# Performance work log

Measured on AMD Instinct MI355X. Metric: run time of the kernel, lower is better.

## Reference

```python
import jax, jax.numpy as jnp
import numpy as np

N_NODES = 100000
IN_DIM = 500
HID_DIM = 128
OUT_DIM = 40
N_EDGES = 1600000


def setup_inputs() -> dict:
    key = jax.random.key(0)
    k1, k2, k3, k4, k5 = jax.random.split(key, 5)
    x = jax.random.normal(k1, (N_NODES, IN_DIM), dtype=jnp.float32)
    edge_index = jax.random.randint(k2, (2, N_EDGES), 0, N_NODES, dtype=jnp.int64)
    # Glorot-style init for linear weights, zero bias (as in PyG GCNConv)
    W1 = jax.random.normal(k3, (IN_DIM, HID_DIM), dtype=jnp.float32) / np.sqrt(IN_DIM)
    b1 = jnp.zeros((HID_DIM,), dtype=jnp.float32)
    W2 = jax.random.normal(k4, (HID_DIM, OUT_DIM), dtype=jnp.float32) / np.sqrt(HID_DIM)
    b2 = jnp.zeros((OUT_DIM,), dtype=jnp.float32)
    return {"x": x, "edge_index": edge_index, "W1": W1, "b1": b1, "W2": W2, "b2": b2}


def reference(x, edge_index, W1, b1, W2, b2):
    N = x.shape[0]
    # GCNConv: add self-loops, symmetric normalization deg^-1/2 A deg^-1/2
    loops = jnp.arange(N, dtype=edge_index.dtype)
    src = jnp.concatenate([edge_index[0], loops])  # [E+N]
    dst = jnp.concatenate([edge_index[1], loops])  # [E+N]
    deg = jax.ops.segment_sum(jnp.ones_like(dst, dtype=x.dtype), dst, num_segments=N)
    dinv = jnp.where(deg > 0, jax.lax.rsqrt(deg), 0.0)
    norm = (dinv[src] * dinv[dst])[:, None]  # [E+N, 1]

    def gcn_conv(h, W, b):
        h = h @ W                              # [N, F_out] linear first (PyG order)
        msg = h[src] * norm                    # gather + scale: [E+N, F_out]
        agg = jax.ops.segment_sum(msg, dst, num_segments=N)  # scatter-add
        return agg + b

    h = jax.nn.relu(gcn_conv(x, W1, b1))
    # dropout(p=0.5) is identity in eval mode
    h = gcn_conv(h, W2, b2)
    return jax.nn.log_softmax(h, axis=1)
```

## Files before the change

kernel.cpp:

```cpp
#include <hip/hip_runtime.h>
#include <hip/hip_bf16.h>

#define IN_DIM 500
#define HID 128
#define OUTD 40
#define KPAD 512

typedef __bf16 bf16x8 __attribute__((ext_vector_type(8)));
typedef float f32x16 __attribute__((ext_vector_type(16)));

static __device__ __forceinline__ float rsqrt_acc(float x) {
  float r = rsqrtf(x);
  return r * (1.5f - 0.5f * x * r * r);
}

static __device__ __forceinline__ unsigned short bf16_of(float f) {
  __bf16 h = (__bf16)f;
  return __builtin_bit_cast(unsigned short, h);
}
static __device__ __forceinline__ float bf16_back(unsigned short u) {
  return (float)__builtin_bit_cast(__bf16, u);
}

__global__ void zero_kernel(int* __restrict__ p, int n) {
  int i = blockIdx.x * 256 + threadIdx.x;
  if (i < n) p[i] = 0;
}

__global__ void hist_kernel(const int* __restrict__ dst, int* __restrict__ deg, int E) {
  int e = blockIdx.x * 256 + threadIdx.x;
  if (e < E) atomicAdd(&deg[dst[e]], 1);
}

__global__ void dinv_kernel(const int* __restrict__ deg, float* __restrict__ dinv, int N) {
  int n = blockIdx.x * 256 + threadIdx.x;
  if (n < N) dinv[n] = rsqrt_acc((float)deg[n] + 1.0f);
}

__global__ void scan_a(const int* __restrict__ deg, int* __restrict__ partial,
                       int* __restrict__ blockSums, int N) {
  __shared__ int sums[256];
  int t = threadIdx.x;
  int base = blockIdx.x * 1024 + t * 4;
  int v0 = (base + 0) < N ? deg[base + 0] : 0;
  int v1 = (base + 1) < N ? deg[base + 1] : 0;
  int v2 = (base + 2) < N ? deg[base + 2] : 0;
  int v3 = (base + 3) < N ? deg[base + 3] : 0;
  int l0 = v0, l1 = l0 + v1, l2 = l1 + v2, l3 = l2 + v3;
  sums[t] = l3;
  __syncthreads();
  for (int o = 1; o < 256; o <<= 1) {
    int a = sums[t];
    int b = (t >= o) ? sums[t - o] : 0;
    __syncthreads();
    sums[t] = a + b;
    __syncthreads();
  }
  int excl = sums[t] - l3;
  if (t == 0) blockSums[blockIdx.x] = sums[255];
  if (base + 0 < N) partial[base + 0] = excl;
  if (base + 1 < N) partial[base + 1] = excl + l0;
  if (base + 2 < N) partial[base + 2] = excl + l1;
  if (base + 3 < N) partial[base + 3] = excl + l2;
}

__global__ void scan_b(int* __restrict__ blockSums, int nb) {
  __shared__ int s[256];
  int t = threadIdx.x;
  int orig = (t < nb) ? blockSums[t] : 0;
  s[t] = orig;
  __syncthreads();
  for (int o = 1; o < 256; o <<= 1) {
    int a = s[t];
    int b = (t >= o) ? s[t - o] : 0;
    __syncthreads();
    s[t] = a + b;
    __syncthreads();
  }
  if (t < nb) blockSums[t] = s[t] - orig;
}

__global__ void scan_c(int* __restrict__ row_ptr, const int* __restrict__ blockOff,
                       int* __restrict__ cursor, int N, int E) {
  int n = blockIdx.x * 256 + threadIdx.x;
  if (n < N) {
    int v = row_ptr[n] + blockOff[n >> 10];
    row_ptr[n] = v;
    cursor[n] = v;
  }
  if (n == 0 && blockIdx.x == 0) row_ptr[N] = E;
}

__global__ void place_kernel(const int* __restrict__ src, const int* __restrict__ dst,
                             const float* __restrict__ dinv, int* __restrict__ cursor,
                             int2* __restrict__ ePair, int E) {
  int e = blockIdx.x * 256 + threadIdx.x;
  if (e < E) {
    int s = src[e], d = dst[e];
    int pos = atomicAdd(&cursor[d], 1);
    int2 rec;
    rec.x = s;
    rec.y = __float_as_int(dinv[s] * dinv[d]);
    ePair[pos] = rec;
  }
}

__global__ void convW1_kernel(const float* __restrict__ W1, unsigned short* __restrict__ Whi,
                              unsigned short* __restrict__ Wlo) {
  int idx = blockIdx.x * 256 + threadIdx.x;
  if (idx >= HID * KPAD) return;
  int n = idx >> 9, k = idx & (KPAD - 1);
  float f = (k < IN_DIM) ? W1[(size_t)k * HID + n] : 0.f;
  unsigned short h = bf16_of(f);
  Whi[idx] = h;
  Wlo[idx] = bf16_of(f - bf16_back(h));
}

#define LSTR 40

__global__ __launch_bounds__(256) void gemm1_kernel(const float* __restrict__ X,
                                                    const unsigned short* __restrict__ Whi,
                                                    const unsigned short* __restrict__ Wlo,
                                                    float* __restrict__ H1, int N) {
  __shared__ unsigned short sAhi[64 * LSTR];
  __shared__ unsigned short sAlo[64 * LSTR];
  __shared__ unsigned short sBhi[128 * LSTR];
  __shared__ unsigned short sBlo[128 * LSTR];
  const int t = threadIdx.x;
  const int rowBase = blockIdx.x * 64;
  const int lane = t & 63;
  const int w = t >> 6;
  const int rw = w & 1;
  const int cw = w >> 1;
  const int m = lane & 31;
  const int quad = lane >> 5;

  f32x16 acc[2];
  acc[0] = (f32x16)(0.f);
  acc[1] = (f32x16)(0.f);

  const int arow = t >> 2;
  const int akoff = (t & 3) * 8;
  const bool arok = (rowBase + arow) < N;
  const float* xrow = X + (size_t)(rowBase + (arok ? arow : 0)) * IN_DIM;
  const int brow = t >> 1;
  const int bkoff = (t & 1) * 16;

  for (int k0 = 0; k0 < KPAD; k0 += 32) {
    __syncthreads();
    {
      float f[8];
      if (arok && (k0 + akoff + 8) <= IN_DIM) {
        const float4* p = (const float4*)(xrow + k0 + akoff);
        float4 v0 = p[0], v1 = p[1];
        f[0] = v0.x; f[1] = v0.y; f[2] = v0.z; f[3] = v0.w;
        f[4] = v1.x; f[5] = v1.y; f[6] = v1.z; f[7] = v1.w;
      } else {
#pragma unroll
        for (int j = 0; j < 8; j++) {
          int k = k0 + akoff + j;
          f[j] = (arok && k < IN_DIM) ? xrow[k] : 0.f;
        }
      }
#pragma unroll
      for (int g = 0; g < 2; g++) {
        ushort4 h, l;
        h.x = bf16_of(f[g*4+0]); l.x = bf16_of(f[g*4+0] - bf16_back(h.x));
        h.y = bf16_of(f[g*4+1]); l.y = bf16_of(f[g*4+1] - bf16_back(h.y));
        h.z = bf16_of(f[g*4+2]); l.z = bf16_of(f[g*4+2] - bf16_back(h.z));
        h.w = bf16_of(f[g*4+3]); l.w = bf16_of(f[g*4+3] - bf16_back(h.w));
        *(ushort4*)&sAhi[arow * LSTR + akoff + g * 4] = h;
        *(ushort4*)&sAlo[arow * LSTR + akoff + g * 4] = l;
      }
    }
    {
      const size_t gb = (size_t)brow * KPAD + k0 + bkoff;
      uint4 h0 = *(const uint4*)&Whi[gb];
      uint4 h1v = *(const uint4*)&Whi[gb + 8];
      uint4 l0 = *(const uint4*)&Wlo[gb];
      uint4 l1 = *(const uint4*)&Wlo[gb + 8];
      *(uint4*)&sBhi[brow * LSTR + bkoff] = h0;
      *(uint4*)&sBhi[brow * LSTR + bkoff + 8] = h1v;
      *(uint4*)&sBlo[brow * LSTR + bkoff] = l0;
      *(uint4*)&sBlo[brow * LSTR + bkoff + 8] = l1;
    }
    __syncthreads();

#pragma unroll
    for (int sub = 0; sub < 2; sub++) {
      const int ks = sub * 16 + quad * 8;
      bf16x8 ah = *(const bf16x8*)&sAhi[(rw * 32 + m) * LSTR + ks];
      bf16x8 al = *(const bf16x8*)&sAlo[(rw * 32 + m) * LSTR + ks];
#pragma unroll
      for (int nt = 0; nt < 2; nt++) {
        bf16x8 bhv = *(const bf16x8*)&sBhi[(cw * 64 + nt * 32 + m) * LSTR + ks];
        bf16x8 blv = *(const bf16x8*)&sBlo[(cw * 64 + nt * 32 + m) * LSTR + ks];
        acc[nt] = __builtin_amdgcn_mfma_f32_32x32x16_bf16(ah, bhv, acc[nt], 0, 0, 0);
        acc[nt] = __builtin_amdgcn_mfma_f32_32x32x16_bf16(ah, blv, acc[nt], 0, 0, 0);
        acc[nt] = __builtin_amdgcn_mfma_f32_32x32x16_bf16(al, bhv, acc[nt], 0, 0, 0);
      }
    }
  }

#pragma unroll
  for (int nt = 0; nt < 2; nt++) {
#pragma unroll
    for (int r = 0; r < 16; r++) {
      int rowin = (r & 3) + 8 * (r >> 2) + 4 * quad;
      int grow = rowBase + rw * 32 + rowin;
      if (grow < N) H1[(size_t)grow * HID + cw * 64 + nt * 32 + m] = acc[nt][r];
    }
  }
}

__global__ void agg1_kernel(const float* __restrict__ h1, const int* __restrict__ row_ptr,
                            const int2* __restrict__ ePair, const float* __restrict__ dinv,
                            const float* __restrict__ b1, float* __restrict__ hrelu, int N) {
  int gid = blockIdx.x * 256 + threadIdx.x;
  int n = gid >> 5, c4 = (gid & 31) * 4;
  if (n >= N) return;
  float di = dinv[n];
  float sl = di * di;
  float4 acc = *(const float4*)&h1[(size_t)n * HID + c4];
  acc.x *= sl; acc.y *= sl; acc.z *= sl; acc.w *= sl;
  int i = row_ptr[n];
  const int s1 = row_ptr[n + 1];
  for (; i + 4 <= s1; i += 4) {
    int2 e0 = ePair[i], e1 = ePair[i + 1], e2 = ePair[i + 2], e3 = ePair[i + 3];
    float w0 = __int_as_float(e0.y), w1 = __int_as_float(e1.y);
    float w2 = __int_as_float(e2.y), w3 = __int_as_float(e3.y);
    float4 v0 = *(const float4*)&h1[(size_t)e0.x * HID + c4];
    float4 v1 = *(const float4*)&h1[(size_t)e1.x * HID + c4];
    float4 v2 = *(const float4*)&h1[(size_t)e2.x * HID + c4];
    float4 v3 = *(const float4*)&h1[(size_t)e3.x * HID + c4];
    acc.x += w0 * v0.x + w1 * v1.x + w2 * v2.x + w3 * v3.x;
    acc.y += w0 * v0.y + w1 * v1.y + w2 * v2.y + w3 * v3.y;
    acc.z += w0 * v0.z + w1 * v1.z + w2 * v2.z + w3 * v3.z;
    acc.w += w0 * v0.w + w1 * v1.w + w2 * v2.w + w3 * v3.w;
  }
  for (; i < s1; i++) {
    int2 e = ePair[i];
    float w = __int_as_float(e.y);
    float4 v = *(const float4*)&h1[(size_t)e.x * HID + c4];
    acc.x += w * v.x; acc.y += w * v.y; acc.z += w * v.z; acc.w += w * v.w;
  }
  float4 bb = *(const float4*)&b1[c4];
  float4 r;
  r.x = fmaxf(acc.x + bb.x, 0.f);
  r.y = fmaxf(acc.y + bb.y, 0.f);
  r.z = fmaxf(acc.z + bb.z, 0.f);
  r.w = fmaxf(acc.w + bb.w, 0.f);
  *(float4*)&hrelu[(size_t)n * HID + c4] = r;
}

__global__ __launch_bounds__(256) void gemm2_kernel(const float* __restrict__ A,
                                                    const float* __restrict__ W2,
                                                    float* __restrict__ H2, int N) {
  __shared__ float tA[64 * 129];
  __shared__ float w2s[128 * 48];
  const int t = threadIdx.x;
  const int rowBase = blockIdx.x * 64;
  for (int idx = t; idx < 128 * 48; idx += 256) {
    int k = idx / 48, c = idx - k * 48;
    w2s[idx] = (c < OUTD) ? W2[k * OUTD + c] : 0.f;
  }
  for (int f = t; f < 2048; f += 256) {
    int row = f >> 5, c4 = (f & 31) * 4;
    float4 v = make_float4(0.f, 0.f, 0.f, 0.f);
    if (rowBase + row < N) v = *(const float4*)&A[(size_t)(rowBase + row) * HID + c4];
    tA[row * 129 + c4 + 0] = v.x;
    tA[row * 129 + c4 + 1] = v.y;
    tA[row * 129 + c4 + 2] = v.z;
    tA[row * 129 + c4 + 3] = v.w;
  }
  __syncthreads();
  const int row = t >> 2;
  const int c0 = (t & 3) * 12;
  float acc[12];
#pragma unroll
  for (int j = 0; j < 12; j++) acc[j] = 0.f;
  for (int k = 0; k < HID; k++) {
    float a = tA[row * 129 + k];
    const float* bp = &w2s[k * 48 + c0];
#pragma unroll
    for (int j = 0; j < 12; j++) acc[j] += a * bp[j];
  }
  int r = rowBase + row;
  if (r < N) {
#pragma unroll
    for (int j = 0; j < 12; j++) {
      int c = c0 + j;
      if (c < OUTD) H2[(size_t)r * OUTD + c] = acc[j];
    }
  }
}

__global__ void agg2_kernel(const float* __restrict__ h2, const int* __restrict__ row_ptr,
                            const int2* __restrict__ ePair, const float* __restrict__ dinv,
                            const float* __restrict__ b2, float* __restrict__ out, int N) {
  int gid = blockIdx.x * 256 + threadIdx.x;
  int n = gid / 10;
  int c4 = (gid - n * 10) * 4;
  if (n >= N) return;
  float di = dinv[n];
  float sl = di * di;
  float4 acc = *(const float4*)&h2[(size_t)n * OUTD + c4];
  acc.x *= sl; acc.y *= sl; acc.z *= sl; acc.w *= sl;
  int i = row_ptr[n];
  const int s1 = row_ptr[n + 1];
  for (; i + 4 <= s1; i += 4) {
    int2 e0 = ePair[i], e1 = ePair[i + 1], e2 = ePair[i + 2], e3 = ePair[i + 3];
    float w0 = __int_as_float(e0.y), w1 = __int_as_float(e1.y);
    float w2 = __int_as_float(e2.y), w3 = __int_as_float(e3.y);
    float4 v0 = *(const float4*)&h2[(size_t)e0.x * OUTD + c4];
    float4 v1 = *(const float4*)&h2[(size_t)e1.x * OUTD + c4];
    float4 v2 = *(const float4*)&h2[(size_t)e2.x * OUTD + c4];
    float4 v3 = *(const float4*)&h2[(size_t)e3.x * OUTD + c4];
    acc.x += w0 * v0.x + w1 * v1.x + w2 * v2.x + w3 * v3.x;
    acc.y += w0 * v0.y + w1 * v1.y + w2 * v2.y + w3 * v3.y;
    acc.z += w0 * v0.z + w1 * v1.z + w2 * v2.z + w3 * v3.z;
    acc.w += w0 * v0.w + w1 * v1.w + w2 * v2.w + w3 * v3.w;
  }
  for (; i < s1; i++) {
    int2 e = ePair[i];
    float w = __int_as_float(e.y);
    float4 v = *(const float4*)&h2[(size_t)e.x * OUTD + c4];
    acc.x += w * v.x; acc.y += w * v.y; acc.z += w * v.z; acc.w += w * v.w;
  }
  float* o = &out[(size_t)n * OUTD + c4];
  o[0] = acc.x + b2[c4 + 0];
  o[1] = acc.y + b2[c4 + 1];
  o[2] = acc.z + b2[c4 + 2];
  o[3] = acc.w + b2[c4 + 3];
}

__global__ void lsm_kernel(float* __restrict__ out, int N) {
  int n = blockIdx.x * 256 + threadIdx.x;
  if (n >= N) return;
  float* row = out + (size_t)n * OUTD;
  float v[OUTD];
  float m = -3.4e38f;
#pragma unroll
  for (int j = 0; j < OUTD; j++) {
    v[j] = row[j];
    m = fmaxf(m, v[j]);
  }
  float s = 0.f;
#pragma unroll
  for (int j = 0; j < OUTD; j++) s += expf(v[j] - m);
  float lse = m + logf(s);
#pragma unroll
  for (int j = 0; j < OUTD; j++) row[j] = v[j] - lse;
}

extern "C" void kernel_launch(void* const* d_in, const int* in_sizes, int n_in,
                              void* d_out, int out_size, void* d_ws, size_t ws_size,
                              hipStream_t stream) {
  const float* x  = (const float*)d_in[0];
  const int*   ei = (const int*)d_in[1];
  const float* W1 = (const float*)d_in[2];
  const float* b1 = (const float*)d_in[3];
  const float* W2 = (const float*)d_in[4];
  const float* b2 = (const float*)d_in[5];
  float* out = (float*)d_out;

  const int N = in_sizes[0] / IN_DIM;
  const int E = in_sizes[1] / 2;
  const int* src = ei;
  const int* dst = ei + E;

  char* wsb = (char*)d_ws;
  size_t off = 0;
  auto alloc = [&](size_t bytes) -> char* {
    char* p = wsb + off;
    off = (off + bytes + 1023) & ~(size_t)1023;
    return p;
  };
  int*   deg       = (int*)alloc((size_t)N * 4);
  float* dinv      = (float*)alloc((size_t)N * 4);
  int*   blockSums = (int*)alloc(1024);
  int*   row_ptr   = (int*)alloc((size_t)(N + 1) * 4);
  int*   cursor    = (int*)alloc((size_t)N * 4);
  int2*  ePair     = (int2*)alloc((size_t)E * 8);
  unsigned short* Whi = (unsigned short*)alloc((size_t)HID * KPAD * 2);
  unsigned short* Wlo = (unsigned short*)alloc((size_t)HID * KPAD * 2);
  float* h1        = (float*)alloc((size_t)N * HID * 4);
  float* hrelu     = (float*)alloc((size_t)N * HID * 4);
  float* h2        = h1;
  (void)n_in; (void)out_size;

  if (off > ws_size) return;

  const int gE = (E + 255) / 256;
  const int gN = (N + 255) / 256;
  const int nb = (N + 1023) / 1024;

  zero_kernel<<<gN, 256, 0, stream>>>(deg, N);
  hist_kernel<<<gE, 256, 0, stream>>>(dst, deg, E);
  dinv_kernel<<<gN, 256, 0, stream>>>(deg, dinv, N);
  scan_a<<<nb, 256, 0, stream>>>(deg, row_ptr, blockSums, N);
  scan_b<<<1, 256, 0, stream>>>(blockSums, nb);
  scan_c<<<gN, 256, 0, stream>>>(row_ptr, blockSums, cursor, N, E);
  place_kernel<<<gE, 256, 0, stream>>>(src, dst, dinv, cursor, ePair, E);
  convW1_kernel<<<(HID * KPAD + 255) / 256, 256, 0, stream>>>(W1, Whi, Wlo);

  gemm1_kernel<<<(N + 63) / 64, 256, 0, stream>>>(x, Whi, Wlo, h1, N);
  agg1_kernel<<<(N * 32 + 255) / 256, 256, 0, stream>>>(h1, row_ptr, ePair, dinv, b1, hrelu, N);
  gemm2_kernel<<<(N + 63) / 64, 256, 0, stream>>>(hrelu, W2, h2, N);
  agg2_kernel<<<(N * 10 + 255) / 256, 256, 0, stream>>>(h2, row_ptr, ePair, dinv, b2, out, N);
  lsm_kernel<<<gN, 256, 0, stream>>>(out, N);
}
```

Measured before the change: 725.8 us.

## Store intermediate node features in fp16 to halve gather traffic

The intermediate activations h1, hrelu and h2 are now stored as fp16 instead of fp32, while accumulation stays in fp32. Agg1 is rewritten so each thread handles 8 fp16 channels, using 16 threads per node instead of 32. The aim is to halve the bytes moved by the random-gather aggregation kernels and by the GEMM stores and loads. The cost is reduced precision in intermediates, with fp16 range and rounding error that could matter for the tolerance check.

```diff
diff --git a/kernel.cpp b/kernel.cpp
--- a/kernel.cpp
+++ b/kernel.cpp
@@ -8,6 +8,8 @@
 
 typedef __bf16 bf16x8 __attribute__((ext_vector_type(8)));
 typedef float f32x16 __attribute__((ext_vector_type(16)));
+typedef unsigned short u16x8 __attribute__((ext_vector_type(8)));
+typedef unsigned short u16x4 __attribute__((ext_vector_type(4)));
 
 static __device__ __forceinline__ float rsqrt_acc(float x) {
   float r = rsqrtf(x);
@@ -20,6 +22,13 @@
 }
 static __device__ __forceinline__ float bf16_back(unsigned short u) {
   return (float)__builtin_bit_cast(__bf16, u);
+}
+static __device__ __forceinline__ unsigned short h16_of(float f) {
+  _Float16 h = (_Float16)f;
+  return __builtin_bit_cast(unsigned short, h);
+}
+static __device__ __forceinline__ float h16_back(unsigned short u) {
+  return (float)__builtin_bit_cast(_Float16, u);
 }
 
 __global__ void zero_kernel(int* __restrict__ p, int n) {
@@ -121,7 +130,7 @@
 __global__ __launch_bounds__(256) void gemm1_kernel(const float* __restrict__ X,
                                                     const unsigned short* __restrict__ Whi,
                                                     const unsigned short* __restrict__ Wlo,
-                                                    float* __restrict__ H1, int N) {
+                                                    unsigned short* __restrict__ H1, int N) {
   __shared__ unsigned short sAhi[64 * LSTR];
   __shared__ unsigned short sAlo[64 * LSTR];
   __shared__ unsigned short sBhi[128 * LSTR];
@@ -208,54 +217,58 @@
     for (int r = 0; r < 16; r++) {
       int rowin = (r & 3) + 8 * (r >> 2) + 4 * quad;
       int grow = rowBase + rw * 32 + rowin;
-      if (grow < N) H1[(size_t)grow * HID + cw * 64 + nt * 32 + m] = acc[nt][r];
-    }
-  }
-}
-
-__global__ void agg1_kernel(const float* __restrict__ h1, const int* __restrict__ row_ptr,
+      if (grow < N) H1[(size_t)grow * HID + cw * 64 + nt * 32 + m] = h16_of(acc[nt][r]);
+    }
+  }
+}
+
+__global__ void agg1_kernel(const unsigned short* __restrict__ h1, const int* __restrict__ row_ptr,
                             const int2* __restrict__ ePair, const float* __restrict__ dinv,
-                            const float* __restrict__ b1, float* __restrict__ hrelu, int N) {
+                            const float* __restrict__ b1, unsigned short* __restrict__ hrelu, int N) {
   int gid = blockIdx.x * 256 + threadIdx.x;
-  int n = gid >> 5, c4 = (gid & 31) * 4;
+  int n = gid >> 4, c8 = (gid & 15) * 8;
   if (n >= N) return;
   float di = dinv[n];
   float sl = di * di;
-  float4 acc = *(const float4*)&h1[(size_t)n * HID + c4];
-  acc.x *= sl; acc.y *= sl; acc.z *= sl; acc.w *= sl;
+  float acc[8];
+  u16x8 sv = *(const u16x8*)&h1[(size_t)n * HID + c8];
+#pragma unroll
+  for (int j = 0; j < 8; j++) acc[j] = sl * h16_back(sv[j]);
   int i = row_ptr[n];
   const int s1 = row_ptr[n + 1];
   for (; i + 4 <= s1; i += 4) {
     int2 e0 = ePair[i], e1 = ePair[i + 1], e2 = ePair[i + 2], e3 = ePair[i + 3];
     float w0 = __int_as_float(e0.y), w1 = __int_as_float(e1.y);
     float w2 = __int_as_float(e2.y), w3 = __int_as_float(e3.y);
-    float4 v0 = *(const float4*)&h1[(size_t)e0.x * HID + c4];
-    float4 v1 = *(const float4*)&h1[(size_t)e1.x * HID + c4];
-    float4 v2 = *(const float4*)&h1[(size_t)e2.x * HID + c4];
-    float4 v3 = *(const float4*)&h1[(size_t)e3.x * HID + c4];
-    acc.x += w0 * v0.x + w1 * v1.x + w2 * v2.x + w3 * v3.x;
-    acc.y += w0 * v0.y + w1 * v1.y + w2 * v2.y + w3 * v3.y;
-    acc.z += w0 * v0.z + w1 * v1.z + w2 * v2.z + w3 * v3.z;
-    acc.w += w0 * v0.w + w1 * v1.w + w2 * v2.w + w3 * v3.w;
+    u16x8 v0 = *(const u16x8*)&h1[(size_t)e0.x * HID + c8];
+    u16x8 v1 = *(const u16x8*)&h1[(size_t)e1.x * HID + c8];
+    u16x8 v2 = *(const u16x8*)&h1[(size_t)e2.x * HID + c8];
+    u16x8 v3 = *(const u16x8*)&h1[(size_t)e3.x * HID + c8];
+#pragma unroll
+    for (int j = 0; j < 8; j++) {
+      acc[j] += w0 * h16_back(v0[j]) + w1 * h16_back(v1[j]) +
+                w2 * h16_back(v2[j]) + w3 * h16_back(v3[j]);
+    }
   }
   for (; i < s1; i++) {
     int2 e = ePair[i];
     float w = __int_as_float(e.y);
-    float4 v = *(const float4*)&h1[(size_t)e.x * HID + c4];
-    acc.x += w * v.x; acc.y += w * v.y; acc.z += w * v.z; acc.w += w * v.w;
-  }
-  float4 bb = *(const float4*)&b1[c4];
-  float4 r;
-  r.x = fmaxf(acc.x + bb.x, 0.f);
-  r.y = fmaxf(acc.y + bb.y, 0.f);
-  r.z = fmaxf(acc.z + bb.z, 0.f);
-  r.w = fmaxf(acc.w + bb.w, 0.f);
-  *(float4*)&hrelu[(size_t)n * HID + c4] = r;
-}
-
-__global__ __launch_bounds__(256) void gemm2_kernel(const float* __restrict__ A,
+    u16x8 v = *(const u16x8*)&h1[(size_t)e.x * HID + c8];
+#pragma unroll
+    for (int j = 0; j < 8; j++) acc[j] += w * h16_back(v[j]);
+  }
+  u16x8 r;
+#pragma unroll
+  for (int j = 0; j < 8; j++) {
+    float v = fmaxf(acc[j] + b1[c8 + j], 0.f);
+    r[j] = h16_of(v);
+  }
+  *(u16x8*)&hrelu[(size_t)n * HID + c8] = r;
+}
+
+__global__ __launch_bounds__(256) void gemm2_kernel(const unsigned short* __restrict__ A,
                                                     const float* __restrict__ W2,
-                                                    float* __restrict__ H2, int N) {
+                                                    unsigned short* __restrict__ H2, int N) {
   __shared__ float tA[64 * 129];
   __shared__ float w2s[128 * 48];
   const int t = threadIdx.x;
@@ -264,14 +277,12 @@
     int k = idx / 48, c = idx - k * 48;
     w2s[idx] = (c < OUTD) ? W2[k * OUTD + c] : 0.f;
   }
-  for (int f = t; f < 2048; f += 256) {
-    int row = f >> 5, c4 = (f & 31) * 4;
-    float4 v = make_float4(0.f, 0.f, 0.f, 0.f);
-    if (rowBase + row < N) v = *(const float4*)&A[(size_t)(rowBase + row) * HID + c4];
-    tA[row * 129 + c4 + 0] = v.x;
-    tA[row * 129 + c4 + 1] = v.y;
-    tA[row * 129 + c4 + 2] = v.z;
-    tA[row * 129 + c4 + 3] = v.w;
+  for (int f = t; f < 1024; f += 256) {
+    int row = f >> 4, c8 = (f & 15) * 8;
+    u16x8 v = (u16x8)(0);
+    if (rowBase + row < N) v = *(const u16x8*)&A[(size_t)(rowBase + row) * HID + c8];
+#pragma unroll
+    for (int j = 0; j < 8; j++) tA[row * 129 + c8 + j] = h16_back(v[j]);
   }
   __syncthreads();
   const int row = t >> 2;
@@ -290,12 +301,12 @@
 #pragma unroll
     for (int j = 0; j < 12; j++) {
       int c = c0 + j;
-      if (c < OUTD) H2[(size_t)r * OUTD + c] = acc[j];
-    }
-  }
-}
-
-__global__ void agg2_kernel(const float* __restrict__ h2, const int* __restrict__ row_ptr,
+      if (c < OUTD) H2[(size_t)r * OUTD + c] = h16_of(acc[j]);
+    }
+  }
+}
+
+__global__ void agg2_kernel(const unsigned short* __restrict__ h2, const int* __restrict__ row_ptr,
                             const int2* __restrict__ ePair, const float* __restrict__ dinv,
                             const float* __restrict__ b2, float* __restrict__ out, int N) {
   int gid = blockIdx.x * 256 + threadIdx.x;
@@ -304,34 +315,36 @@
   if (n >= N) return;
   float di = dinv[n];
   float sl = di * di;
-  float4 acc = *(const float4*)&h2[(size_t)n * OUTD + c4];
-  acc.x *= sl; acc.y *= sl; acc.z *= sl; acc.w *= sl;
+  float acc[4];
+  u16x4 sv = *(const u16x4*)&h2[(size_t)n * OUTD + c4];
+#pragma unroll
+  for (int j = 0; j < 4; j++) acc[j] = sl * h16_back(sv[j]);
   int i = row_ptr[n];
   const int s1 = row_ptr[n + 1];
   for (; i + 4 <= s1; i += 4) {
     int2 e0 = ePair[i], e1 = ePair[i + 1], e2 = ePair[i + 2], e3 = ePair[i + 3];
     float w0 = __int_as_float(e0.y), w1 = __int_as_float(e1.y);
     float w2 = __int_as_float(e2.y), w3 = __int_as_float(e3.y);
-    float4 v0 = *(const float4*)&h2[(size_t)e0.x * OUTD + c4];
-    float4 v1 = *(const float4*)&h2[(size_t)e1.x * OUTD + c4];
-    float4 v2 = *(const float4*)&h2[(size_t)e2.x * OUTD + c4];
-    float4 v3 = *(const float4*)&h2[(size_t)e3.x * OUTD + c4];
-    acc.x += w0 * v0.x + w1 * v1.x + w2 * v2.x + w3 * v3.x;
-    acc.y += w0 * v0.y + w1 * v1.y + w2 * v2.y + w3 * v3.y;
-    acc.z += w0 * v0.z + w1 * v1.z + w2 * v2.z + w3 * v3.z;
-    acc.w += w0 * v0.w + w1 * v1.w + w2 * v2.w + w3 * v3.w;
+    u16x4 v0 = *(const u16x4*)&h2[(size_t)e0.x * OUTD + c4];
+    u16x4 v1 = *(const u16x4*)&h2[(size_t)e1.x * OUTD + c4];
+    u16x4 v2 = *(const u16x4*)&h2[(size_t)e2.x * OUTD + c4];
+    u16x4 v3 = *(const u16x4*)&h2[(size_t)e3.x * OUTD + c4];
+#pragma unroll
+    for (int j = 0; j < 4; j++) {
+      acc[j] += w0 * h16_back(v0[j]) + w1 * h16_back(v1[j]) +
+                w2 * h16_back(v2[j]) + w3 * h16_back(v3[j]);
+    }
   }
   for (; i < s1; i++) {
     int2 e = ePair[i];
     float w = __int_as_float(e.y);
-    float4 v = *(const float4*)&h2[(size_t)e.x * OUTD + c4];
-    acc.x += w * v.x; acc.y += w * v.y; acc.z += w * v.z; acc.w += w * v.w;
+    u16x4 v = *(const u16x4*)&h2[(size_t)e.x * OUTD + c4];
+#pragma unroll
+    for (int j = 0; j < 4; j++) acc[j] += w * h16_back(v[j]);
   }
   float* o = &out[(size_t)n * OUTD + c4];
-  o[0] = acc.x + b2[c4 + 0];
-  o[1] = acc.y + b2[c4 + 1];
-  o[2] = acc.z + b2[c4 + 2];
-  o[3] = acc.w + b2[c4 + 3];
+#pragma unroll
+  for (int j = 0; j < 4; j++) o[j] = acc[j] + b2[c4 + j];
 }
 
 __global__ void lsm_kernel(float* __restrict__ out, int N) {
@@ -384,9 +397,9 @@
   int2*  ePair     = (int2*)alloc((size_t)E * 8);
   unsigned short* Whi = (unsigned short*)alloc((size_t)HID * KPAD * 2);
   unsigned short* Wlo = (unsigned short*)alloc((size_t)HID * KPAD * 2);
-  float* h1        = (float*)alloc((size_t)N * HID * 4);
-  float* hrelu     = (float*)alloc((size_t)N * HID * 4);
-  float* h2        = h1;
+  unsigned short* h1h    = (unsigned short*)alloc((size_t)N * HID * 2);
+  unsigned short* hreluh = (unsigned short*)alloc((size_t)N * HID * 2);
+  unsigned short* h2h    = h1h;
   (void)n_in; (void)out_size;
 
   if (off > ws_size) return;
@@ -404,9 +417,9 @@
   place_kernel<<<gE, 256, 0, stream>>>(src, dst, dinv, cursor, ePair, E);
   convW1_kernel<<<(HID * KPAD + 255) / 256, 256, 0, stream>>>(W1, Whi, Wlo);
 
-  gemm1_kernel<<<(N + 63) / 64, 256, 0, stream>>>(x, Whi, Wlo, h1, N);
-  agg1_kernel<<<(N * 32 + 255) / 256, 256, 0, stream>>>(h1, row_ptr, ePair, dinv, b1, hrelu, N);
-  gemm2_kernel<<<(N + 63) / 64, 256, 0, stream>>>(hrelu, W2, h2, N);
-  agg2_kernel<<<(N * 10 + 255) / 256, 256, 0, stream>>>(h2, row_ptr, ePair, dinv, b2, out, N);
+  gemm1_kernel<<<(N + 63) / 64, 256, 0, stream>>>(x, Whi, Wlo, h1h, N);
+  agg1_kernel<<<(N * 16 + 255) / 256, 256, 0, stream>>>(h1h, row_ptr, ePair, dinv, b1, hreluh, N);
+  gemm2_kernel<<<(N + 63) / 64, 256, 0, stream>>>(hreluh, W2, h2h, N);
+  agg2_kernel<<<(N * 10 + 255) / 256, 256, 0, stream>>>(h2h, row_ptr, ePair, dinv, b2, out, N);
   lsm_kernel<<<gN, 256, 0, stream>>>(out, N);
 }
```

New measurement: 640.8 us. -11.7%, faster.
